# Performance work log

Hardware: AMD Instinct MI355X
Metric: run time of the kernel (lower is better)

Reference implementation:

```python
import jax, jax.numpy as jnp
import numpy as np

EMBED = 1024
HEADS = 16
HEAD_DIM = EMBED // HEADS


def setup_inputs() -> dict:
    key = jax.random.key(0)
    ks = jax.random.split(key, 8)
    N, L = 2, 2048
    values = jax.random.normal(ks[0], (N, L, EMBED), dtype=jnp.float32)
    keys_ = jax.random.normal(ks[1], (N, L, EMBED), dtype=jnp.float32)
    query = jax.random.normal(ks[2], (N, L, EMBED), dtype=jnp.float32)
    mask = jnp.ones((N, 1, 1, L), dtype=jnp.int32)
    s = 1.0 / np.sqrt(EMBED)
    W_q = jax.random.normal(ks[3], (EMBED, EMBED), dtype=jnp.float32) * s
    W_k = jax.random.normal(ks[4], (EMBED, EMBED), dtype=jnp.float32) * s
    W_v = jax.random.normal(ks[5], (EMBED, EMBED), dtype=jnp.float32) * s
    W_o = jax.random.normal(ks[6], (EMBED, EMBED), dtype=jnp.float32) * s
    b_o = jax.random.normal(ks[7], (EMBED,), dtype=jnp.float32) * 0.01
    return {"values": values, "keys": keys_, "query": query, "mask": mask,
            "W_q": W_q, "W_k": W_k, "W_v": W_v, "W_o": W_o, "b_o": b_o}


def reference(values, keys, query, mask, W_q, W_k, W_v, W_o, b_o):
    N, Lq, _ = query.shape
    Lk = keys.shape[1]
    # projections (torch Linear: x @ W.T); reshape to (N, H, L, Dh)
    q = (query @ W_q.T).reshape(N, Lq, HEADS, HEAD_DIM).transpose(0, 2, 1, 3)
    k = (keys @ W_k.T).reshape(N, Lk, HEADS, HEAD_DIM).transpose(0, 2, 1, 3)
    v = (values @ W_v.T).reshape(N, Lk, HEADS, HEAD_DIM).transpose(0, 2, 1, 3)
    energy = jnp.einsum('bhqd,bhkd->bhqk', q, k) / jnp.sqrt(jnp.float32(HEAD_DIM))
    energy = jnp.where(mask == 0, jnp.float32(-1e20), energy)
    attn = jax.nn.softmax(energy, axis=-1)
    out = jnp.einsum('bhqk,bhkd->bhqd', attn, v)
    out = out.transpose(0, 2, 1, 3).reshape(N, Lq, EMBED)
    return out @ W_o.T + b_o
```

## Files before the change

kernel.cpp:

```cpp
#include <hip/hip_runtime.h>
#include <cstddef>
#include <cstdint>

#define SEQ    2048
#define NBATCH 2

typedef unsigned short u16;
typedef unsigned int   u32;
typedef __attribute__((ext_vector_type(8))) short bf16x8;
typedef __attribute__((ext_vector_type(4))) float f32x4;

#if __has_builtin(__builtin_amdgcn_exp2f)
#define EXP2F(x) __builtin_amdgcn_exp2f(x)
#else
#define EXP2F(x) exp2f(x)
#endif

#define GLL16(g, l) __builtin_amdgcn_global_load_lds( \
    (const __attribute__((address_space(1))) void*)(g), \
    (__attribute__((address_space(3))) void*)(l), 16, 0, 0)

__device__ __forceinline__ u32 fbits(float x) { union { float f; u32 u; } c; c.f = x; return c.u; }
__device__ __forceinline__ u16 f2bf(float x) { return (u16)((fbits(x) + 0x8000u) >> 16); }
__device__ __forceinline__ u32 pack2bf(float lo, float hi) {
    return __builtin_amdgcn_perm(fbits(hi) + 0x8000u, fbits(lo) + 0x8000u, 0x07060302u);
}

__global__ __launch_bounds__(256)
void cast_all(const float* __restrict__ q, const float* __restrict__ k, const float* __restrict__ v,
              const float* __restrict__ wq, const float* __restrict__ wk,
              const float* __restrict__ wv, const float* __restrict__ wo,
              u16* __restrict__ oq, u16* __restrict__ ok, u16* __restrict__ ov,
              u16* __restrict__ owq, u16* __restrict__ owk, u16* __restrict__ owv,
              u16* __restrict__ owo)
{
    const float* s; u16* d; int i;
    if (blockIdx.y == 0)      { s = q; d = oq; i = blockIdx.x * 256 + threadIdx.x; }
    else if (blockIdx.y == 1) { s = k; d = ok; i = blockIdx.x * 256 + threadIdx.x; }
    else if (blockIdx.y == 2) { s = v; d = ov; i = blockIdx.x * 256 + threadIdx.x; }
    else {
        const int w = blockIdx.x >> 10, xi = blockIdx.x & 1023;
        if (w == 0)      { s = wq; d = owq; }
        else if (w == 1) { s = wk; d = owk; }
        else if (w == 2) { s = wv; d = owv; }
        else             { s = wo; d = owo; }
        i = xi * 256 + threadIdx.x;
    }
    float4 vv = ((const float4*)s)[i];
    uint2 r; r.x = pack2bf(vv.x, vv.y); r.y = pack2bf(vv.z, vv.w);
    ((uint2*)d)[i] = r;
}

__device__ __forceinline__
void gemm_body(const u16* __restrict__ X, const u16* __restrict__ W,
               void* __restrict__ Yv, const int layout)
{
    __shared__ u16 smem[16896];
    u16* As = smem;
    u16* Bs = smem + 8192;

    const int tid  = threadIdx.x;
    const int wave = tid >> 6;
    const int lane = tid & 63;
    const int lm   = lane & 15;
    const int quad = lane >> 4;
    const int m0 = blockIdx.x * 128;
    const int n0 = blockIdx.y * 128;
    const int wr = (wave & 1) * 64;
    const int wc = (wave >> 1) * 64;

    const int srow = wave * 32 + (lane >> 3);
    const int scol = (lane & 7) * 8;
    const u16* xg = X + (size_t)(m0 + srow) * 1024 + scol;
    const u16* wg = W + (size_t)(n0 + srow) * 1024 + scol;

    f32x4 acc[4][4] = {};

    for (int k0 = 0; k0 < 1024; k0 += 64) {
        __syncthreads();
        #pragma unroll
        for (int p = 0; p < 4; ++p) {
            GLL16(xg + k0 + p * 8 * 1024, &As[(wave * 32 + p * 8) * 64]);
            GLL16(wg + k0 + p * 8 * 1024, &Bs[(wave * 32 + p * 8) * 64]);
        }
        __syncthreads();
        #pragma unroll
        for (int kk = 0; kk < 64; kk += 32) {
            bf16x8 af[4], bf[4];
            #pragma unroll
            for (int t = 0; t < 4; ++t) {
                af[t] = *(const bf16x8*)&As[(wr + t * 16 + lm) * 64 + kk + quad * 8];
                bf[t] = *(const bf16x8*)&Bs[(wc + t * 16 + lm) * 64 + kk + quad * 8];
            }
            #pragma unroll
            for (int i = 0; i < 4; ++i)
                #pragma unroll
                for (int j = 0; j < 4; ++j)
                    acc[i][j] = __builtin_amdgcn_mfma_f32_16x16x32_bf16(af[i], bf[j], acc[i][j], 0, 0, 0);
        }
    }

    if (layout == 0) {
        u16* Y = (u16*)Yv;
        #pragma unroll
        for (int i = 0; i < 4; ++i)
            #pragma unroll
            for (int j = 0; j < 4; ++j) {
                const int C = n0 + wc + j * 16 + lm;
                #pragma unroll
                for (int r = 0; r < 4; ++r) {
                    const int R = m0 + wr + i * 16 + quad * 4 + r;
                    Y[(size_t)R * 1024 + C] = f2bf(acc[i][j][r]);
                }
            }
    } else {
        __syncthreads();
        u16* T = smem;
        #pragma unroll
        for (int i = 0; i < 4; ++i)
            #pragma unroll
            for (int j = 0; j < 4; ++j) {
                const int col = wc + j * 16 + lm;
                const int row = wr + i * 16 + quad * 4;
                uint2 v;
                v.x = pack2bf(acc[i][j][0], acc[i][j][1]);
                v.y = pack2bf(acc[i][j][2], acc[i][j][3]);
                *(uint2*)&T[col * 132 + row] = v;
            }
        __syncthreads();
        const int dp = tid >> 1, half = (tid & 1) * 64;
        const int nn = m0 >> 11, l0 = m0 & 2047;
        const int C = n0 + dp, h = C >> 6, d = C & 63;
        u16* Y = (u16*)Yv;
        const size_t base = (((size_t)nn * 16 + h) * 64 + d) * SEQ + l0 + half;
        #pragma unroll
        for (int p = 0; p < 8; ++p) {
            bf16x8 v = *(const bf16x8*)&T[dp * 132 + half + p * 8];
            *(bf16x8*)(Y + base + p * 8) = v;
        }
    }
}

__global__ __launch_bounds__(256, 3)
void gemm_qkv(const u16* __restrict__ xq, const u16* __restrict__ xk, const u16* __restrict__ xv,
              const u16* __restrict__ wq, const u16* __restrict__ wk, const u16* __restrict__ wv,
              u16* __restrict__ qb, u16* __restrict__ kb, u16* __restrict__ vt)
{
    if (blockIdx.z == 0)      gemm_body(xq, wq, qb, 0);
    else if (blockIdx.z == 1) gemm_body(xk, wk, kb, 0);
    else                      gemm_body(xv, wv, vt, 2);
}

__global__ __launch_bounds__(256, 2)
void gemm_out64(const u16* __restrict__ X, const u16* __restrict__ W,
                float* __restrict__ Y, const float* __restrict__ bias)
{
    __shared__ u16 As[128 * 64];
    __shared__ u16 Bs[64 * 64];

    const int tid  = threadIdx.x;
    const int wave = tid >> 6;
    const int lane = tid & 63;
    const int lm   = lane & 15;
    const int quad = lane >> 4;
    const int m0 = blockIdx.x * 128;
    const int n0 = blockIdx.y * 64;
    const int wr = (wave & 1) * 64;
    const int wc = (wave >> 1) * 32;

    const int sr8 = lane >> 3, sc8 = (lane & 7) * 8;
    const u16* xg = X + (size_t)(m0 + wave * 32 + sr8) * 1024 + sc8;
    const u16* wg = W + (size_t)(n0 + wave * 16 + sr8) * 1024 + sc8;

    f32x4 acc[4][2] = {};

    for (int k0 = 0; k0 < 1024; k0 += 64) {
        __syncthreads();
        #pragma unroll
        for (int p = 0; p < 4; ++p)
            GLL16(xg + k0 + p * 8 * 1024, &As[(wave * 32 + p * 8) * 64]);
        #pragma unroll
        for (int p = 0; p < 2; ++p)
            GLL16(wg + k0 + p * 8 * 1024, &Bs[(wave * 16 + p * 8) * 64]);
        __syncthreads();
        #pragma unroll
        for (int kk = 0; kk < 64; kk += 32) {
            bf16x8 af[4], bf[2];
            #pragma unroll
            for (int t = 0; t < 4; ++t)
                af[t] = *(const bf16x8*)&As[(wr + t * 16 + lm) * 64 + kk + quad * 8];
            #pragma unroll
            for (int j = 0; j < 2; ++j)
                bf[j] = *(const bf16x8*)&Bs[(wc + j * 16 + lm) * 64 + kk + quad * 8];
            #pragma unroll
            for (int i = 0; i < 4; ++i)
                #pragma unroll
                for (int j = 0; j < 2; ++j)
                    acc[i][j] = __builtin_amdgcn_mfma_f32_16x16x32_bf16(af[i], bf[j], acc[i][j], 0, 0, 0);
        }
    }

    #pragma unroll
    for (int i = 0; i < 4; ++i)
        #pragma unroll
        for (int j = 0; j < 2; ++j) {
            const int C = n0 + wc + j * 16 + lm;
            const float bv = bias[C];
            #pragma unroll
            for (int r = 0; r < 4; ++r) {
                const int R = m0 + wr + i * 16 + quad * 4 + r;
                Y[(size_t)R * 1024 + C] = acc[i][j][r] + bv;
            }
        }
}

__global__ __launch_bounds__(256, 2)
void flash_attn_bf16(const u16* __restrict__ Qb, const u16* __restrict__ Kb,
                     const u16* __restrict__ VT, const int* __restrict__ mask,
                     u16* __restrict__ O)
{
    __shared__ u16 Ks[128 * 72];
    __shared__ u16 Vts[64 * 136];
    __shared__ u16 Ps[4][32 * 72];

    const int tid  = threadIdx.x;
    const int wave = tid >> 6;
    const int lane = tid & 63;
    const int lm   = lane & 15;
    const int quad = lane >> 4;

    const int wid = blockIdx.x + 16 * blockIdx.y + 256 * blockIdx.z;
    const int idx = wid >> 3;
    const int hn  = (wid & 7) + 8 * (idx & 3);
    const int h   = hn & 15, n = hn >> 4;
    const int wq  = (idx >> 2) * 128 + wave * 32;

    const u16* Qh = Qb + ((size_t)n * SEQ) * 1024 + h * 64;
    const u16* Kh = Kb + ((size_t)n * SEQ) * 1024 + h * 64;
    const u16* Vh = VT + (((size_t)n * 16 + h) * 64) * SEQ;
    const int* mk = mask + (size_t)n * SEQ;
    u16* Pw = &Ps[wave][0];

    bf16x8 qf[2][2];
    #pragma unroll
    for (int t = 0; t < 2; ++t)
        #pragma unroll
        for (int s = 0; s < 2; ++s)
            qf[t][s] = *(const bf16x8*)(Qh + (size_t)(wq + t * 16 + lm) * 1024 + s * 32 + quad * 8);

    f32x4 o_acc[2][4] = {};
    float l_i[2][4] = {};

    const int kr = tid >> 1, kc = (tid & 1) * 32;
    const int vr = tid >> 2, vc = (tid & 3) * 32;

    bf16x8 ka[4], va[4];
    #pragma unroll
    for (int p = 0; p < 4; ++p) {
        ka[p] = *(const bf16x8*)(Kh + (size_t)kr * 1024 + kc + p * 8);
        va[p] = *(const bf16x8*)(Vh + (size_t)vr * SEQ + vc + p * 8);
    }

    const float cs = 0.125f * 1.44269504f;

    for (int c0 = 0; c0 < SEQ; c0 += 128) {
        __syncthreads();
        #pragma unroll
        for (int p = 0; p < 4; ++p) {
            *(bf16x8*)&Ks[kr * 72 + kc + p * 8]   = ka[p];
            *(bf16x8*)&Vts[vr * 136 + vc + p * 8] = va[p];
        }
        __syncthreads();

        if (c0 + 128 < SEQ) {
            #pragma unroll
            for (int p = 0; p < 4; ++p) {
                ka[p] = *(const bf16x8*)(Kh + (size_t)(c0 + 128 + kr) * 1024 + kc + p * 8);
                va[p] = *(const bf16x8*)(Vh + (size_t)vr * SEQ + c0 + 128 + vc + p * 8);
            }
        }

        f32x4 s[2][8] = {};
        #pragma unroll
        for (int nt = 0; nt < 8; ++nt) {
            bf16x8 kf0 = *(const bf16x8*)&Ks[(nt * 16 + lm) * 72 + quad * 8];
            bf16x8 kf1 = *(const bf16x8*)&Ks[(nt * 16 + lm) * 72 + 32 + quad * 8];
            #pragma unroll
            for (int t = 0; t < 2; ++t) {
                s[t][nt] = __builtin_amdgcn_mfma_f32_16x16x32_bf16(qf[t][0], kf0, s[t][nt], 0, 0, 0);
                s[t][nt] = __builtin_amdgcn_mfma_f32_16x16x32_bf16(qf[t][1], kf1, s[t][nt], 0, 0, 0);
            }
        }

        int msk[8];
        #pragma unroll
        for (int nt = 0; nt < 8; ++nt) msk[nt] = mk[c0 + nt * 16 + lm];
        #pragma unroll
        for (int t = 0; t < 2; ++t)
            #pragma unroll
            for (int nt = 0; nt < 8; ++nt)
                #pragma unroll
                for (int r = 0; r < 4; ++r) {
                    float e = EXP2F(s[t][nt][r] * cs);
                    e = msk[nt] ? e : 0.0f;
                    s[t][nt][r] = e;
                    l_i[t][r] += e;
                }

        #pragma unroll
        for (int half = 0; half < 2; ++half) {
            #pragma unroll
            for (int t = 0; t < 2; ++t)
                #pragma unroll
                for (int ntl = 0; ntl < 4; ++ntl)
                    #pragma unroll
                    for (int r = 0; r < 4; ++r)
                        Pw[(t * 16 + quad * 4 + r) * 72 + ntl * 16 + lm] =
                            f2bf(s[t][half * 4 + ntl][r]);

            #pragma unroll
            for (int ksl = 0; ksl < 2; ++ksl) {
                bf16x8 pf[2];
                #pragma unroll
                for (int t = 0; t < 2; ++t)
                    pf[t] = *(const bf16x8*)&Pw[(t * 16 + lm) * 72 + ksl * 32 + quad * 8];
                #pragma unroll
                for (int dt = 0; dt < 4; ++dt) {
                    bf16x8 vf = *(const bf16x8*)&Vts[(dt * 16 + lm) * 136 + half * 64 + ksl * 32 + quad * 8];
                    #pragma unroll
                    for (int t = 0; t < 2; ++t)
                        o_acc[t][dt] = __builtin_amdgcn_mfma_f32_16x16x32_bf16(pf[t], vf, o_acc[t][dt], 0, 0, 0);
                }
            }
        }
    }

    #pragma unroll
    for (int t = 0; t < 2; ++t)
        #pragma unroll
        for (int r = 0; r < 4; ++r) {
            float v = l_i[t][r];
            #pragma unroll
            for (int off = 1; off < 16; off <<= 1) v += __shfl_xor(v, off);
            l_i[t][r] = 1.0f / v;
        }
    #pragma unroll
    for (int t = 0; t < 2; ++t)
        #pragma unroll
        for (int dt = 0; dt < 4; ++dt)
            #pragma unroll
            for (int r = 0; r < 4; ++r) {
                const int ql = wq + t * 16 + quad * 4 + r;
                const int col = h * 64 + dt * 16 + lm;
                O[((size_t)n * SEQ + ql) * 1024 + col] = f2bf(o_acc[t][dt][r] * l_i[t][r]);
            }
}

extern "C" void kernel_launch(void* const* d_in, const int* in_sizes, int n_in,
                              void* d_out, int out_size, void* d_ws, size_t ws_size,
                              hipStream_t stream)
{
    const float* values = (const float*)d_in[0];
    const float* keys   = (const float*)d_in[1];
    const float* query  = (const float*)d_in[2];
    const int*   mask   = (const int*)d_in[3];
    const float* W_q    = (const float*)d_in[4];
    const float* W_k    = (const float*)d_in[5];
    const float* W_v    = (const float*)d_in[6];
    const float* W_o    = (const float*)d_in[7];
    const float* b_o    = (const float*)d_in[8];

    const size_t NTOK = (size_t)NBATCH * SEQ * 1024;
    const size_t WSZ  = 1024 * 1024;
    u16* p = (u16*)d_ws;
    u16* qb    = p; p += NTOK;
    u16* kb    = p; p += NTOK;
    u16* vt    = p; p += NTOK;
    u16* xq    = p; p += NTOK;
    u16* xk    = p; p += NTOK;
    u16* xv    = p; p += NTOK;
    u16* attnb = p; p += NTOK;
    u16* wqb   = p; p += WSZ;
    u16* wkb   = p; p += WSZ;
    u16* wvb   = p; p += WSZ;
    u16* wob   = p; p += WSZ;

    cast_all<<<dim3(4096, 4), 256, 0, stream>>>(query, keys, values,
                                                W_q, W_k, W_v, W_o,
                                                xq, xk, xv, wqb, wkb, wvb, wob);

    gemm_qkv<<<dim3(32, 8, 3), 256, 0, stream>>>(xq, xk, xv, wqb, wkb, wvb, qb, kb, vt);

    flash_attn_bf16<<<dim3(16, 16, 2), 256, 0, stream>>>(qb, kb, vt, mask, attnb);

    gemm_out64<<<dim3(32, 16), 256, 0, stream>>>(attnb, wob, (float*)d_out, b_o);
}
```

Baseline: 229.7 us.

## Fuse activation bf16 cast into QKV GEMM and transpose attention score MFMA

Drops the separate cast of the query, key and value activations. The QKV GEMM now loads fp32 activations into registers, converts them to bf16 and stores them in padded LDS, prefetching the next K tile while the current one is computed, which removes a full write and re-read of three bf16 activation tensors. In flash attention the score MFMA operands are swapped, so each lane holds four consecutive keys for a single query. This allows vectorized mask loads, packed 8-byte P stores to LDS, and one row sum per query tile in place of four. The risks are extra register pressure in the GEMM and synchronous fp32 global loads in place of async direct-to-LDS loads.

```diff
diff --git a/kernel.cpp b/kernel.cpp
--- a/kernel.cpp
+++ b/kernel.cpp
@@ -27,37 +27,30 @@
 }
 
 __global__ __launch_bounds__(256)
-void cast_all(const float* __restrict__ q, const float* __restrict__ k, const float* __restrict__ v,
-              const float* __restrict__ wq, const float* __restrict__ wk,
-              const float* __restrict__ wv, const float* __restrict__ wo,
-              u16* __restrict__ oq, u16* __restrict__ ok, u16* __restrict__ ov,
-              u16* __restrict__ owq, u16* __restrict__ owk, u16* __restrict__ owv,
-              u16* __restrict__ owo)
-{
-    const float* s; u16* d; int i;
-    if (blockIdx.y == 0)      { s = q; d = oq; i = blockIdx.x * 256 + threadIdx.x; }
-    else if (blockIdx.y == 1) { s = k; d = ok; i = blockIdx.x * 256 + threadIdx.x; }
-    else if (blockIdx.y == 2) { s = v; d = ov; i = blockIdx.x * 256 + threadIdx.x; }
-    else {
-        const int w = blockIdx.x >> 10, xi = blockIdx.x & 1023;
-        if (w == 0)      { s = wq; d = owq; }
-        else if (w == 1) { s = wk; d = owk; }
-        else if (w == 2) { s = wv; d = owv; }
-        else             { s = wo; d = owo; }
-        i = xi * 256 + threadIdx.x;
-    }
+void cast_w(const float* __restrict__ wq, const float* __restrict__ wk,
+            const float* __restrict__ wv, const float* __restrict__ wo,
+            u16* __restrict__ owq, u16* __restrict__ owk,
+            u16* __restrict__ owv, u16* __restrict__ owo)
+{
+    const int w = blockIdx.x >> 10, xi = blockIdx.x & 1023;
+    const float* s; u16* d;
+    if (w == 0)      { s = wq; d = owq; }
+    else if (w == 1) { s = wk; d = owk; }
+    else if (w == 2) { s = wv; d = owv; }
+    else             { s = wo; d = owo; }
+    const int i = xi * 256 + threadIdx.x;
     float4 vv = ((const float4*)s)[i];
     uint2 r; r.x = pack2bf(vv.x, vv.y); r.y = pack2bf(vv.z, vv.w);
     ((uint2*)d)[i] = r;
 }
 
 __device__ __forceinline__
-void gemm_body(const u16* __restrict__ X, const u16* __restrict__ W,
-               void* __restrict__ Yv, const int layout)
-{
-    __shared__ u16 smem[16896];
+void gemm_body_f32A(const float* __restrict__ X, const u16* __restrict__ W,
+                    void* __restrict__ Yv, const int layout)
+{
+    __shared__ u16 smem[128 * 72 + 128 * 64];
     u16* As = smem;
-    u16* Bs = smem + 8192;
+    u16* Bs = smem + 128 * 72;
 
     const int tid  = threadIdx.x;
     const int wave = tid >> 6;
@@ -69,10 +62,16 @@
     const int wr = (wave & 1) * 64;
     const int wc = (wave >> 1) * 64;
 
-    const int srow = wave * 32 + (lane >> 3);
-    const int scol = (lane & 7) * 8;
-    const u16* xg = X + (size_t)(m0 + srow) * 1024 + scol;
-    const u16* wg = W + (size_t)(n0 + srow) * 1024 + scol;
+    const int srow = tid >> 1;
+    const int scol = (tid & 1) * 32;
+    const float* xg = X + (size_t)(m0 + srow) * 1024 + scol;
+    const int brow = wave * 32 + (lane >> 3);
+    const int bcol = (lane & 7) * 8;
+    const u16* wg = W + (size_t)(n0 + brow) * 1024 + bcol;
+
+    float4 pa[8];
+    #pragma unroll
+    for (int p = 0; p < 8; ++p) pa[p] = ((const float4*)xg)[p];
 
     f32x4 acc[4][4] = {};
 
@@ -80,16 +79,25 @@
         __syncthreads();
         #pragma unroll
         for (int p = 0; p < 4; ++p) {
-            GLL16(xg + k0 + p * 8 * 1024, &As[(wave * 32 + p * 8) * 64]);
+            const float4 a = pa[2 * p], b = pa[2 * p + 1];
+            union { u32 w[4]; bf16x8 v; } u;
+            u.w[0] = pack2bf(a.x, a.y); u.w[1] = pack2bf(a.z, a.w);
+            u.w[2] = pack2bf(b.x, b.y); u.w[3] = pack2bf(b.z, b.w);
+            *(bf16x8*)&As[srow * 72 + scol + p * 8] = u.v;
             GLL16(wg + k0 + p * 8 * 1024, &Bs[(wave * 32 + p * 8) * 64]);
         }
         __syncthreads();
+        if (k0 + 64 < 1024) {
+            #pragma unroll
+            for (int p = 0; p < 8; ++p)
+                pa[p] = ((const float4*)(xg + k0 + 64))[p];
+        }
         #pragma unroll
         for (int kk = 0; kk < 64; kk += 32) {
             bf16x8 af[4], bf[4];
             #pragma unroll
             for (int t = 0; t < 4; ++t) {
-                af[t] = *(const bf16x8*)&As[(wr + t * 16 + lm) * 64 + kk + quad * 8];
+                af[t] = *(const bf16x8*)&As[(wr + t * 16 + lm) * 72 + kk + quad * 8];
                 bf[t] = *(const bf16x8*)&Bs[(wc + t * 16 + lm) * 64 + kk + quad * 8];
             }
             #pragma unroll
@@ -142,13 +150,13 @@
 }
 
 __global__ __launch_bounds__(256, 3)
-void gemm_qkv(const u16* __restrict__ xq, const u16* __restrict__ xk, const u16* __restrict__ xv,
+void gemm_qkv(const float* __restrict__ q, const float* __restrict__ k, const float* __restrict__ v,
               const u16* __restrict__ wq, const u16* __restrict__ wk, const u16* __restrict__ wv,
               u16* __restrict__ qb, u16* __restrict__ kb, u16* __restrict__ vt)
 {
-    if (blockIdx.z == 0)      gemm_body(xq, wq, qb, 0);
-    else if (blockIdx.z == 1) gemm_body(xk, wk, kb, 0);
-    else                      gemm_body(xv, wv, vt, 2);
+    if (blockIdx.z == 0)      gemm_body_f32A(q, wq, qb, 0);
+    else if (blockIdx.z == 1) gemm_body_f32A(k, wk, kb, 0);
+    else                      gemm_body_f32A(v, wv, vt, 2);
 }
 
 __global__ __launch_bounds__(256, 2)
@@ -229,7 +237,7 @@
     const int lm   = lane & 15;
     const int quad = lane >> 4;
 
-    const int wid = blockIdx.x + 16 * blockIdx.y + 256 * blockIdx.z;
+    const int wid = blockIdx.x;
     const int idx = wid >> 3;
     const int hn  = (wid & 7) + 8 * (idx & 3);
     const int h   = hn & 15, n = hn >> 4;
@@ -243,13 +251,13 @@
 
     bf16x8 qf[2][2];
     #pragma unroll
-    for (int t = 0; t < 2; ++t)
+    for (int qt = 0; qt < 2; ++qt)
         #pragma unroll
         for (int s = 0; s < 2; ++s)
-            qf[t][s] = *(const bf16x8*)(Qh + (size_t)(wq + t * 16 + lm) * 1024 + s * 32 + quad * 8);
+            qf[qt][s] = *(const bf16x8*)(Qh + (size_t)(wq + qt * 16 + lm) * 1024 + s * 32 + quad * 8);
 
     f32x4 o_acc[2][4] = {};
-    float l_i[2][4] = {};
+    float l_i[2] = {};
 
     const int kr = tid >> 1, kc = (tid & 1) * 32;
     const int vr = tid >> 2, vc = (tid & 3) * 32;
@@ -280,79 +288,82 @@
             }
         }
 
-        f32x4 s[2][8] = {};
-        #pragma unroll
-        for (int nt = 0; nt < 8; ++nt) {
-            bf16x8 kf0 = *(const bf16x8*)&Ks[(nt * 16 + lm) * 72 + quad * 8];
-            bf16x8 kf1 = *(const bf16x8*)&Ks[(nt * 16 + lm) * 72 + 32 + quad * 8];
-            #pragma unroll
-            for (int t = 0; t < 2; ++t) {
-                s[t][nt] = __builtin_amdgcn_mfma_f32_16x16x32_bf16(qf[t][0], kf0, s[t][nt], 0, 0, 0);
-                s[t][nt] = __builtin_amdgcn_mfma_f32_16x16x32_bf16(qf[t][1], kf1, s[t][nt], 0, 0, 0);
-            }
-        }
-
-        int msk[8];
-        #pragma unroll
-        for (int nt = 0; nt < 8; ++nt) msk[nt] = mk[c0 + nt * 16 + lm];
-        #pragma unroll
-        for (int t = 0; t < 2; ++t)
-            #pragma unroll
-            for (int nt = 0; nt < 8; ++nt)
-                #pragma unroll
-                for (int r = 0; r < 4; ++r) {
-                    float e = EXP2F(s[t][nt][r] * cs);
-                    e = msk[nt] ? e : 0.0f;
-                    s[t][nt][r] = e;
-                    l_i[t][r] += e;
+        int4 mkv[8];
+        #pragma unroll
+        for (int kt = 0; kt < 8; ++kt)
+            mkv[kt] = *(const int4*)(mk + c0 + kt * 16 + quad * 4);
+
+        f32x4 st[8][2] = {};
+        #pragma unroll
+        for (int kt = 0; kt < 8; ++kt) {
+            bf16x8 kf0 = *(const bf16x8*)&Ks[(kt * 16 + lm) * 72 + quad * 8];
+            bf16x8 kf1 = *(const bf16x8*)&Ks[(kt * 16 + lm) * 72 + 32 + quad * 8];
+            #pragma unroll
+            for (int qt = 0; qt < 2; ++qt) {
+                st[kt][qt] = __builtin_amdgcn_mfma_f32_16x16x32_bf16(kf0, qf[qt][0], st[kt][qt], 0, 0, 0);
+                st[kt][qt] = __builtin_amdgcn_mfma_f32_16x16x32_bf16(kf1, qf[qt][1], st[kt][qt], 0, 0, 0);
+            }
+        }
+
+        #pragma unroll
+        for (int half = 0; half < 2; ++half) {
+            #pragma unroll
+            for (int ktl = 0; ktl < 4; ++ktl) {
+                const int kt = half * 4 + ktl;
+                const int4 mv = mkv[kt];
+                const int mm[4] = {mv.x, mv.y, mv.z, mv.w};
+                #pragma unroll
+                for (int qt = 0; qt < 2; ++qt) {
+                    float e[4];
+                    #pragma unroll
+                    for (int r = 0; r < 4; ++r) {
+                        float v = EXP2F(st[kt][qt][r] * cs);
+                        v = mm[r] ? v : 0.0f;
+                        e[r] = v;
+                        l_i[qt] += v;
+                    }
+                    uint2 w;
+                    w.x = pack2bf(e[0], e[1]);
+                    w.y = pack2bf(e[2], e[3]);
+                    *(uint2*)&Pw[(qt * 16 + lm) * 72 + ktl * 16 + quad * 4] = w;
                 }
-
-        #pragma unroll
-        for (int half = 0; half < 2; ++half) {
-            #pragma unroll
-            for (int t = 0; t < 2; ++t)
-                #pragma unroll
-                for (int ntl = 0; ntl < 4; ++ntl)
-                    #pragma unroll
-                    for (int r = 0; r < 4; ++r)
-                        Pw[(t * 16 + quad * 4 + r) * 72 + ntl * 16 + lm] =
-                            f2bf(s[t][half * 4 + ntl][r]);
-
+            }
             #pragma unroll
             for (int ksl = 0; ksl < 2; ++ksl) {
                 bf16x8 pf[2];
                 #pragma unroll
-                for (int t = 0; t < 2; ++t)
-                    pf[t] = *(const bf16x8*)&Pw[(t * 16 + lm) * 72 + ksl * 32 + quad * 8];
+                for (int qt = 0; qt < 2; ++qt)
+                    pf[qt] = *(const bf16x8*)&Pw[(qt * 16 + lm) * 72 + ksl * 32 + quad * 8];
                 #pragma unroll
                 for (int dt = 0; dt < 4; ++dt) {
                     bf16x8 vf = *(const bf16x8*)&Vts[(dt * 16 + lm) * 136 + half * 64 + ksl * 32 + quad * 8];
                     #pragma unroll
-                    for (int t = 0; t < 2; ++t)
-                        o_acc[t][dt] = __builtin_amdgcn_mfma_f32_16x16x32_bf16(pf[t], vf, o_acc[t][dt], 0, 0, 0);
+                    for (int qt = 0; qt < 2; ++qt)
+                        o_acc[qt][dt] = __builtin_amdgcn_mfma_f32_16x16x32_bf16(pf[qt], vf, o_acc[qt][dt], 0, 0, 0);
                 }
             }
         }
     }
 
-    #pragma unroll
-    for (int t = 0; t < 2; ++t)
-        #pragma unroll
-        for (int r = 0; r < 4; ++r) {
-            float v = l_i[t][r];
-            #pragma unroll
-            for (int off = 1; off < 16; off <<= 1) v += __shfl_xor(v, off);
-            l_i[t][r] = 1.0f / v;
-        }
-    #pragma unroll
-    for (int t = 0; t < 2; ++t)
+    float linv[2][4];
+    #pragma unroll
+    for (int qt = 0; qt < 2; ++qt) {
+        float v = l_i[qt];
+        v += __shfl_xor(v, 16);
+        v += __shfl_xor(v, 32);
+        #pragma unroll
+        for (int r = 0; r < 4; ++r)
+            linv[qt][r] = 1.0f / __shfl(v, quad * 4 + r);
+    }
+    #pragma unroll
+    for (int qt = 0; qt < 2; ++qt)
         #pragma unroll
         for (int dt = 0; dt < 4; ++dt)
             #pragma unroll
             for (int r = 0; r < 4; ++r) {
-                const int ql = wq + t * 16 + quad * 4 + r;
+                const int ql = wq + qt * 16 + quad * 4 + r;
                 const int col = h * 64 + dt * 16 + lm;
-                O[((size_t)n * SEQ + ql) * 1024 + col] = f2bf(o_acc[t][dt][r] * l_i[t][r]);
+                O[((size_t)n * SEQ + ql) * 1024 + col] = f2bf(o_acc[qt][dt][r] * linv[qt][r]);
             }
 }
 
@@ -376,22 +387,18 @@
     u16* qb    = p; p += NTOK;
     u16* kb    = p; p += NTOK;
     u16* vt    = p; p += NTOK;
-    u16* xq    = p; p += NTOK;
-    u16* xk    = p; p += NTOK;
-    u16* xv    = p; p += NTOK;
     u16* attnb = p; p += NTOK;
     u16* wqb   = p; p += WSZ;
     u16* wkb   = p; p += WSZ;
     u16* wvb   = p; p += WSZ;
     u16* wob   = p; p += WSZ;
 
-    cast_all<<<dim3(4096, 4), 256, 0, stream>>>(query, keys, values,
-                                                W_q, W_k, W_v, W_o,
-                                                xq, xk, xv, wqb, wkb, wvb, wob);
-
-    gemm_qkv<<<dim3(32, 8, 3), 256, 0, stream>>>(xq, xk, xv, wqb, wkb, wvb, qb, kb, vt);
-
-    flash_attn_bf16<<<dim3(16, 16, 2), 256, 0, stream>>>(qb, kb, vt, mask, attnb);
+    cast_w<<<4096, 256, 0, stream>>>(W_q, W_k, W_v, W_o, wqb, wkb, wvb, wob);
+
+    gemm_qkv<<<dim3(32, 8, 3), 256, 0, stream>>>(query, keys, values,
+                                                 wqb, wkb, wvb, qb, kb, vt);
+
+    flash_attn_bf16<<<512, 256, 0, stream>>>(qb, kb, vt, mask, attnb);
 
     gemm_out64<<<dim3(32, 16), 256, 0, stream>>>(attnb, wob, (float*)d_out, b_o);
 }
```

Result: slower. 246.2 us (+7.2%).
